# Optimization experiments

Hardware: AMD Instinct MI355X
Metric: run time of the kernel (lower is better)

## Reference

```python
import jax, jax.numpy as jnp
import numpy as np

L = 32768      # sequence length
H = 512        # n_features == d_model
P = 128        # state_size // 2 (conj_sym)
EPS = 1e-5     # haiku LayerNorm default eps


def setup_inputs() -> dict:
    key = jax.random.key(0)
    ks = jax.random.split(key, 10)
    x = jax.random.normal(ks[0], (L, H), dtype=jnp.float32)
    # S5 parameters (HiPPO-like init approximated with random values of same structure)
    lambda_real = -(0.1 + 0.5 * jax.random.uniform(ks[1], (P,), dtype=jnp.float32))
    lambda_imag = jnp.pi * jnp.arange(P, dtype=jnp.float32)
    b = jax.random.normal(ks[2], (P, H, 2), dtype=jnp.float32) / np.sqrt(H)
    c = jax.random.normal(ks[3], (H, P, 2), dtype=jnp.float32) / np.sqrt(2 * P)
    d = jax.random.normal(ks[4], (H,), dtype=jnp.float32)
    # log-uniform timescales in [1e-3, 1e-1]
    u = jax.random.uniform(ks[5], (P, 1), dtype=jnp.float32)
    delta = jnp.log(1e-3) + u * (jnp.log(1e-1) - jnp.log(1e-3))
    norm_scale = jnp.ones((H,), dtype=jnp.float32)
    norm_offset = jnp.zeros((H,), dtype=jnp.float32)
    w2 = jax.random.normal(ks[6], (H, H), dtype=jnp.float32) / np.sqrt(H)
    b2 = jnp.zeros((H,), dtype=jnp.float32)
    return {"x": x, "lambda_real": lambda_real, "lambda_imag": lambda_imag,
            "b": b, "c": c, "d": d, "delta": delta,
            "norm_scale": norm_scale, "norm_offset": norm_offset,
            "w2": w2, "b2": b2}


def _s5_block(x, lambda_real, lambda_imag, b, c, d, delta, norm_scale, norm_offset, w2, b2):
    skip = x
    # prenorm LayerNorm over last axis
    mean = jnp.mean(x, axis=-1, keepdims=True)
    var = jnp.var(x, axis=-1, keepdims=True)
    xn = (x - mean) * jax.lax.rsqrt(var + EPS) * norm_scale + norm_offset

    # --- S5 SSM ---
    lam = lambda_real + 1j * lambda_imag                      # [P]
    B = b[..., 0] + 1j * b[..., 1]                            # [P, H]
    C = c[..., 0] + 1j * c[..., 1]                            # [H, P]
    step = jnp.exp(delta[:, 0])                               # [P] (step_rescale = 1)
    # bilinear discretization
    bl = 1.0 / (1.0 - (step / 2.0) * lam)
    lam_bar = bl * (1.0 + (step / 2.0) * lam)                 # [P]
    B_bar = (bl * step)[:, None] * B                          # [P, H]

    Bu = jnp.einsum('lh,ph->lp', xn.astype(jnp.complex64), B_bar)  # [L, P]
    lam_elems = jnp.broadcast_to(lam_bar, (L, P))

    def binop(qi, qj):
        Ai, bi = qi
        Aj, bj = qj
        return Aj * Ai, Aj * bi + bj

    _, xs = jax.lax.associative_scan(binop, (lam_elems, Bu))  # states [L, P]
    # conj_sym: output is 2 * Re(C x)
    ys = 2.0 * jnp.einsum('lp,hp->lh', xs, C).real            # [L, H]
    y = ys + d * xn                                           # D skip term

    # half_glu2 (dropout_rate = 0 -> identity)
    x1 = jax.nn.gelu(y)
    out = y * jax.nn.sigmoid(x1 @ w2 + b2)
    return skip + out


def reference(x, lambda_real, lambda_imag, b, c, d, delta, norm_scale, norm_offset, w2, b2):
    return _s5_block(x, lambda_real, lambda_imag, b, c, d, delta,
                     norm_scale, norm_offset, w2, b2)
```

## Files before the change

### kernel.cpp

```cpp
#include <hip/hip_runtime.h>
#include <hip/hip_bf16.h>
#include <math.h>

#define LSEQ 32768
#define HF   512
#define PS   128
#define TWOP 256
#define NC   512
#define CL   64

typedef __attribute__((ext_vector_type(8))) short short8v;
typedef __attribute__((ext_vector_type(4))) float f32x4;

__device__ __forceinline__ float sig_fast(float z) {
    return __builtin_amdgcn_rcpf(1.0f + __expf(-z));
}
__device__ __forceinline__ float gelu_fast(float v) {
    float z = 1.5957691216057308f * v * fmaf(0.044715f, v * v, 1.0f);
    return v * sig_fast(z);
}
__device__ __forceinline__ unsigned short bf16bits(float f) {
    __hip_bfloat16 h = __float2bfloat16(f);
    return *(unsigned short*)&h;
}
__device__ __forceinline__ float bf2f(unsigned short u) {
    unsigned v = ((unsigned)u) << 16;
    return *(float*)&v;
}
__device__ __forceinline__ unsigned pk2(float a, float b) {
    return ((unsigned)bf16bits(b) << 16) | bf16bits(a);
}
__device__ __forceinline__ void gload_lds16(const void* g, void* l) {
    __builtin_amdgcn_global_load_lds(
        (const __attribute__((address_space(1))) unsigned int*)g,
        (__attribute__((address_space(3))) unsigned int*)l, 16, 0, 0);
}

__global__ __launch_bounds__(128) void prep_lam_k(
    const float* __restrict__ lr_, const float* __restrict__ li_,
    const float* __restrict__ delta, float* lam, float* bls, float* lamPow)
{
    int p = threadIdx.x;
    float lr = lr_[p], li = li_[p];
    float step = expf(delta[p]);
    float s2 = 0.5f * step;
    float dr = 1.0f - s2 * lr, di = -s2 * li;
    float inv = 1.0f / (dr * dr + di * di);
    float blr = dr * inv, bli = -di * inv;
    float nr = 1.0f + s2 * lr, ni = s2 * li;
    float lbr = blr * nr - bli * ni;
    float lbi = blr * ni + bli * nr;
    lam[2 * p] = lbr; lam[2 * p + 1] = lbi;
    bls[2 * p] = blr * step; bls[2 * p + 1] = bli * step;
    float pr = 1.0f, pim = 0.0f;
    lamPow[2 * p] = 1.0f; lamPow[2 * p + 1] = 0.0f;
    for (int k = 1; k <= CL; k++) {
        float t = pr * lbr - pim * lbi;
        pim = pr * lbi + pim * lbr;
        pr = t;
        lamPow[k * TWOP + 2 * p] = pr;
        lamPow[k * TWOP + 2 * p + 1] = pim;
    }
}

__global__ __launch_bounds__(256) void prep_B_k(
    const float* __restrict__ b, const float* __restrict__ bls,
    unsigned short* __restrict__ bwt)
{
    int idx = blockIdx.x * 256 + threadIdx.x;
    int p = idx >> 9, h = idx & 511;
    float2 bb = *(const float2*)(b + ((size_t)p * HF + h) * 2);
    float sr = bls[2 * p], si = bls[2 * p + 1];
    bwt[(size_t)(2 * p) * HF + h]     = bf16bits(sr * bb.x - si * bb.y);
    bwt[(size_t)(2 * p + 1) * HF + h] = bf16bits(sr * bb.y + si * bb.x);
}

__global__ __launch_bounds__(256) void prep_C_k(
    const float* __restrict__ c, unsigned short* __restrict__ cwt)
{
    int idx = blockIdx.x * 256 + threadIdx.x;
    int h = idx >> 7, p = idx & 127;
    float2 cc = *(const float2*)(c + ((size_t)h * PS + p) * 2);
    *(unsigned*)(cwt + (size_t)h * TWOP + 2 * p) = pk2(2.0f * cc.x, -2.0f * cc.y);
}

__global__ __launch_bounds__(256) void prep_w2_k(
    const float* __restrict__ w2, unsigned short* __restrict__ w2t)
{
    int idx = blockIdx.x * 256 + threadIdx.x;
    int n = idx >> 9, k = idx & 511;
    w2t[(size_t)n * HF + k] = bf16bits(w2[(size_t)k * HF + n]);
}

__global__ __launch_bounds__(128) void ln_k(
    const float* __restrict__ x, const float* __restrict__ scale,
    const float* __restrict__ offs, unsigned short* __restrict__ xnbf)
{
    int row = blockIdx.x, t = threadIdx.x;
    const float4* xr = (const float4*)(x + (size_t)row * HF);
    float4 v = xr[t];
    float s = v.x + v.y + v.z + v.w;
    float q = v.x * v.x + v.y * v.y + v.z * v.z + v.w * v.w;
    #pragma unroll
    for (int off = 32; off > 0; off >>= 1) {
        s += __shfl_down(s, off);
        q += __shfl_down(q, off);
    }
    __shared__ float ss[2], qq[2];
    if ((t & 63) == 0) { ss[t >> 6] = s; qq[t >> 6] = q; }
    __syncthreads();
    float S = ss[0] + ss[1], Q = qq[0] + qq[1];
    float mean = S * (1.0f / HF);
    float var = Q * (1.0f / HF) - mean * mean;
    float rstd = rsqrtf(var + 1e-5f);
    float4 sc = ((const float4*)scale)[t];
    float4 of = ((const float4*)offs)[t];
    ushort4 hv;
    hv.x = bf16bits((v.x - mean) * rstd * sc.x + of.x);
    hv.y = bf16bits((v.y - mean) * rstd * sc.y + of.y);
    hv.z = bf16bits((v.z - mean) * rstd * sc.z + of.z);
    hv.w = bf16bits((v.w - mean) * rstd * sc.w + of.w);
    ((ushort4*)(xnbf + (size_t)row * HF))[t] = hv;
}

__global__ __launch_bounds__(256) void g1scan_k(
    const unsigned short* __restrict__ A,
    const unsigned short* __restrict__ Bt,
    unsigned short* __restrict__ xs16,
    float* __restrict__ F,
    const float* __restrict__ lam)
{
    __shared__ float yt[128 * 128];
    unsigned short* As = (unsigned short*)yt;
    unsigned short* Bs = (unsigned short*)yt + 128 * 32;
    const int K = HF;
    int flat = (blockIdx.y << 1) + blockIdx.x;
    int f2 = (flat & 7) * 64 + (flat >> 3);
    const int bxi = f2 & 1, byi = f2 >> 1;
    const int bm = byi << 7;
    const int bn = bxi << 7;
    const int tid = threadIdx.x;
    const int lane = tid & 63;
    const int wid = tid >> 6;
    const int wr = wid >> 1, wc = wid & 1;

    f32x4 acc[4][4] = {};

    const int r0 = (wid << 5) + (lane >> 2);
    const int c0 = (lane & 3) << 3;
    const unsigned short* gA = A + (size_t)(bm + r0) * K + c0;
    const unsigned short* gB = Bt + (size_t)(bn + r0) * K + c0;
    unsigned short* lA0 = As + (wid << 5) * 32;
    unsigned short* lA1 = As + ((wid << 5) + 16) * 32;
    unsigned short* lB0 = Bs + (wid << 5) * 32;
    unsigned short* lB1 = Bs + ((wid << 5) + 16) * 32;
    const int aoff = ((wr << 6) + (lane & 15)) * 32 + ((lane >> 4) << 3);
    const int boff = ((wc << 6) + (lane & 15)) * 32 + ((lane >> 4) << 3);

    #pragma unroll
    for (int k0 = 0; k0 < HF; k0 += 32) {
        gload_lds16(gA + k0, lA0);
        gload_lds16(gA + k0 + (size_t)16 * K, lA1);
        gload_lds16(gB + k0, lB0);
        gload_lds16(gB + k0 + (size_t)16 * K, lB1);
        __syncthreads();
        short8v a[4], b[4];
        #pragma unroll
        for (int m = 0; m < 4; m++)
            a[m] = *(const short8v*)(As + aoff + (m << 4) * 32);
        #pragma unroll
        for (int n = 0; n < 4; n++)
            b[n] = *(const short8v*)(Bs + boff + (n << 4) * 32);
        #pragma unroll
        for (int m = 0; m < 4; m++)
            #pragma unroll
            for (int n = 0; n < 4; n++)
                acc[m][n] = __builtin_amdgcn_mfma_f32_16x16x32_bf16(
                    a[m], b[n], acc[m][n], 0, 0, 0);
        __syncthreads();
    }

    #pragma unroll
    for (int m = 0; m < 4; m++) {
        const int rowb = (wr << 6) + (m << 4) + ((lane >> 4) << 2);
        #pragma unroll
        for (int n = 0; n < 4; n++) {
            const int col = (wc << 6) + (n << 4) + (lane & 15);
            #pragma unroll
            for (int j = 0; j < 4; j++)
                yt[(rowb + j) * 128 + col] = acc[m][n][j];
        }
    }
    __syncthreads();

    if (tid < 128) {
        int ch = tid >> 6, q = tid & 63;
        int pg = (bxi << 6) + q;
        float lr = lam[2 * pg], liv = lam[2 * pg + 1];
        float sr = 0.0f, si = 0.0f;
        float* col = yt + (ch << 6) * 128 + 2 * q;
        #pragma unroll 8
        for (int i = 0; i < CL; i++) {
            float ur = col[i * 128], ui = col[i * 128 + 1];
            float tr = lr * sr - liv * si + ur;
            float ti = lr * si + liv * sr + ui;
            sr = tr; si = ti;
            col[i * 128] = sr; col[i * 128 + 1] = si;
        }
        int cg = (byi << 1) + ch;
        F[(size_t)cg * TWOP + (bxi << 7) + 2 * q] = sr;
        F[(size_t)cg * TWOP + (bxi << 7) + 2 * q + 1] = si;
    }
    __syncthreads();

    #pragma unroll
    for (int j = 0; j < 8; j++) {
        int fl = j * 256 + tid;
        int r = fl >> 4, ck = fl & 15;
        float4 v0 = *(float4*)&yt[r * 128 + ck * 8];
        float4 v1 = *(float4*)&yt[r * 128 + ck * 8 + 4];
        uint4 o;
        o.x = pk2(v0.x, v0.y); o.y = pk2(v0.z, v0.w);
        o.z = pk2(v1.x, v1.y); o.w = pk2(v1.z, v1.w);
        *(uint4*)(xs16 + (size_t)(bm + r) * TWOP + bn + ck * 8) = o;
    }
}

__global__ __launch_bounds__(512) void carry_k(
    const float* __restrict__ F, float* __restrict__ G,
    const float* __restrict__ lamPow)
{
    __shared__ float2 buf[NC];
    int c = threadIdx.x, p = blockIdx.x;
    float2 f = *(const float2*)(F + (size_t)c * TWOP + 2 * p);
    buf[c] = f;
    float aR = lamPow[CL * TWOP + 2 * p], aI = lamPow[CL * TWOP + 2 * p + 1];
    __syncthreads();
    #pragma unroll
    for (int d = 1; d < NC; d <<= 1) {
        bool act = (c >= d);
        float2 pv = act ? buf[c - d] : make_float2(0.0f, 0.0f);
        __syncthreads();
        if (act) {
            float2 cur = buf[c];
            cur.x += aR * pv.x - aI * pv.y;
            cur.y += aR * pv.y + aI * pv.x;
            buf[c] = cur;
        }
        __syncthreads();
        float nR = aR * aR - aI * aI;
        float nI = 2.0f * aR * aI;
        aR = nR; aI = nI;
    }
    *(float2*)(G + (size_t)c * TWOP + 2 * p) = buf[c];
}

__global__ __launch_bounds__(128) void fix_k(
    const unsigned short* __restrict__ xs16, const float* __restrict__ G,
    const float* __restrict__ lamPow, unsigned short* __restrict__ xsbf)
{
    int bc = blockIdx.x;
    int c = bc >> 2, qq = bc & 3;
    int p = threadIdx.x;
    float gr = 0.0f, gi = 0.0f;
    if (c > 0) {
        float2 g = *(const float2*)(G + (size_t)(c - 1) * TWOP + 2 * p);
        gr = g.x; gi = g.y;
    }
    size_t base = ((size_t)c * CL + (qq << 4)) * TWOP + 2 * p;
    #pragma unroll
    for (int i = 0; i < 16; i++) {
        float2 lp = *(const float2*)(lamPow + (size_t)((qq << 4) + i + 1) * TWOP + 2 * p);
        unsigned u = *(const unsigned*)(xs16 + base + (size_t)i * TWOP);
        float vr = bf2f((unsigned short)(u & 0xffff)) + lp.x * gr - lp.y * gi;
        float vi = bf2f((unsigned short)(u >> 16))    + lp.x * gi + lp.y * gr;
        *(unsigned*)(xsbf + base + (size_t)i * TWOP) = pk2(vr, vi);
    }
}

template<int MODE, int KT, int NT>
__global__ __launch_bounds__(256) void mgemm_k(
    const unsigned short* __restrict__ A, const unsigned short* __restrict__ Bt,
    const float* __restrict__ e0, const unsigned short* __restrict__ e1h,
    const float* __restrict__ e2, float* __restrict__ outF,
    unsigned short* __restrict__ o1, unsigned short* __restrict__ o2)
{
    __shared__ float smem[4224];
    unsigned short* As = (unsigned short*)smem;
    unsigned short* Bs = As + 128 * 32;
    float* eb = smem;

    constexpr int GX = NT >> 7;
    int flat = blockIdx.y * GX + blockIdx.x;
    constexpr int NWG = GX * (LSEQ >> 7);
    int f2 = (flat & 7) * (NWG >> 3) + (flat >> 3);
    const int bm = (f2 / GX) << 7;
    const int bn = (f2 % GX) << 7;

    const int tid = threadIdx.x;
    const int lane = tid & 63;
    const int wid = tid >> 6;
    const int wr = wid >> 1, wc = wid & 1;

    f32x4 acc[4][4] = {};

    const int r0 = (wid << 5) + (lane >> 2);
    const int c0 = (lane & 3) << 3;
    const unsigned short* gA = A + (size_t)(bm + r0) * KT + c0;
    const unsigned short* gB = Bt + (size_t)(bn + r0) * KT + c0;
    unsigned short* lA0 = As + (wid << 5) * 32;
    unsigned short* lA1 = As + ((wid << 5) + 16) * 32;
    unsigned short* lB0 = Bs + (wid << 5) * 32;
    unsigned short* lB1 = Bs + ((wid << 5) + 16) * 32;
    const int aoff = ((wr << 6) + (lane & 15)) * 32 + ((lane >> 4) << 3);
    const int boff = ((wc << 6) + (lane & 15)) * 32 + ((lane >> 4) << 3);

    #pragma unroll
    for (int k0 = 0; k0 < KT; k0 += 32) {
        gload_lds16(gA + k0, lA0);
        gload_lds16(gA + k0 + (size_t)16 * KT, lA1);
        gload_lds16(gB + k0, lB0);
        gload_lds16(gB + k0 + (size_t)16 * KT, lB1);
        __syncthreads();
        short8v a[4], b[4];
        #pragma unroll
        for (int m = 0; m < 4; m++)
            a[m] = *(const short8v*)(As + aoff + (m << 4) * 32);
        #pragma unroll
        for (int n = 0; n < 4; n++)
            b[n] = *(const short8v*)(Bs + boff + (n << 4) * 32);
        #pragma unroll
        for (int m = 0; m < 4; m++)
            #pragma unroll
            for (int n = 0; n < 4; n++)
                acc[m][n] = __builtin_amdgcn_mfma_f32_16x16x32_bf16(
                    a[m], b[n], acc[m][n], 0, 0, 0);
        __syncthreads();
    }

    #pragma unroll
    for (int p = 0; p < 4; p++) {
        if ((p >> 1) == wr) {
            const int mb = (p & 1) << 1;
            #pragma unroll
            for (int mm = 0; mm < 2; mm++) {
                const int lrow = (mm << 4) + ((lane >> 4) << 2);
                #pragma unroll
                for (int n = 0; n < 4; n++) {
                    const int col = (wc << 6) + (n << 4) + (lane & 15);
                    #pragma unroll
                    for (int j = 0; j < 4; j++)
                        eb[(lrow + j) * 132 + col] = acc[mb + mm][n][j];
                }
            }
        }
        __syncthreads();
        #pragma unroll
        for (int i = 0; i < 4; i++) {
            int idx = (i << 8) + tid;
            int row = idx >> 5, c4 = idx & 31;
            int gr = bm + (p << 5) + row;
            int gc = bn + (c4 << 2);
            size_t off = (size_t)gr * NT + gc;
            float4 v = *(float4*)&eb[row * 132 + (c4 << 2)];
            float4 e0v = *(const float4*)(e0 + gc);
            if (MODE == 1) {
                ushort4 xv = *(const ushort4*)(e1h + off);
                float y0 = v.x + e0v.x * bf2f(xv.x);
                float y1 = v.y + e0v.y * bf2f(xv.y);
                float y2 = v.z + e0v.z * bf2f(xv.z);
                float y3 = v.w + e0v.w * bf2f(xv.w);
                ushort4 a1, a2;
                a1.x = bf16bits(y0); a1.y = bf16bits(y1);
                a1.z = bf16bits(y2); a1.w = bf16bits(y3);
                a2.x = bf16bits(gelu_fast(y0)); a2.y = bf16bits(gelu_fast(y1));
                a2.z = bf16bits(gelu_fast(y2)); a2.w = bf16bits(gelu_fast(y3));
                *(ushort4*)(o1 + off) = a1;
                *(ushort4*)(o2 + off) = a2;
            } else {
                ushort4 yv = *(const ushort4*)(e1h + off);
                float4 xv = *(const float4*)(e2 + off);
                float4 o;
                o.x = xv.x + bf2f(yv.x) * sig_fast(v.x + e0v.x);
                o.y = xv.y + bf2f(yv.y) * sig_fast(v.y + e0v.y);
                o.z = xv.z + bf2f(yv.z) * sig_fast(v.z + e0v.z);
                o.w = xv.w + bf2f(yv.w) * sig_fast(v.w + e0v.w);
                *(float4*)(outF + off) = o;
            }
        }
        __syncthreads();
    }
}

extern "C" void kernel_launch(void* const* d_in, const int* in_sizes, int n_in,
                              void* d_out, int out_size, void* d_ws, size_t ws_size,
                              hipStream_t stream)
{
    const float* x      = (const float*)d_in[0];
    const float* lr     = (const float*)d_in[1];
    const float* li     = (const float*)d_in[2];
    const float* b      = (const float*)d_in[3];
    const float* c      = (const float*)d_in[4];
    const float* d      = (const float*)d_in[5];
    const float* delta  = (const float*)d_in[6];
    const float* nsc    = (const float*)d_in[7];
    const float* noff   = (const float*)d_in[8];
    const float* w2     = (const float*)d_in[9];
    const float* b2     = (const float*)d_in[10];
    float* out = (float*)d_out;

    unsigned short* XNBF = (unsigned short*)d_ws;
    unsigned short* YBF  = XNBF + (size_t)LSEQ * HF;
    unsigned short* XS16 = YBF + (size_t)LSEQ * HF;
    unsigned short* XSBF = XS16 + (size_t)LSEQ * TWOP;
    unsigned short* BWT  = XSBF + (size_t)LSEQ * TWOP;
    unsigned short* CWT  = BWT + (size_t)TWOP * HF;
    unsigned short* W2T  = CWT + (size_t)HF * TWOP;
    float* lam    = (float*)(W2T + (size_t)HF * HF);
    float* bls    = lam + TWOP;
    float* lamPow = bls + TWOP;
    float* F      = lamPow + (size_t)(CL + 1) * TWOP;
    float* G      = F + (size_t)NC * TWOP;

    prep_lam_k<<<1, 128, 0, stream>>>(lr, li, delta, lam, bls, lamPow);
    prep_B_k<<<(PS * HF) / 256, 256, 0, stream>>>(b, bls, BWT);
    prep_C_k<<<(HF * PS) / 256, 256, 0, stream>>>(c, CWT);
    prep_w2_k<<<(HF * HF) / 256, 256, 0, stream>>>(w2, W2T);
    ln_k<<<LSEQ, 128, 0, stream>>>(x, nsc, noff, XNBF);
    g1scan_k<<<dim3(TWOP >> 7, LSEQ >> 7), 256, 0, stream>>>(
        XNBF, BWT, XS16, F, lam);
    carry_k<<<PS, 512, 0, stream>>>(F, G, lamPow);
    fix_k<<<NC * 4, 128, 0, stream>>>(XS16, G, lamPow, XSBF);
    mgemm_k<1, TWOP, HF><<<dim3(4, LSEQ >> 7), 256, 0, stream>>>(
        XSBF, CWT, d, XNBF, nullptr, nullptr, YBF, XNBF);
    mgemm_k<2, HF, HF><<<dim3(4, LSEQ >> 7), 256, 0, stream>>>(
        XNBF, W2T, b2, YBF, x, out, nullptr, nullptr);
}
```

Measured before the change: 239.6 us.

## Double-buffer LDS tiles in GEMM main loops to overlap loads with MFMA

Both the Bu-scan GEMM and the generic mgemm kernel now keep two LDS stages. The next K-slice is prefetched with global_load_lds while the current slice is being multiplied, and each step ends with one vmcnt(0) wait plus a barrier instead of two syncthreads. The aim is to hide global-load latency behind MFMA work. The cost is a larger mgemm shared-memory footprint, 32KB versus about 17KB, which may lower occupancy. Correctness relies on the single barrier per step ordering the LDS reads of one buffer before that buffer is overwritten.

```diff
diff --git a/kernel.cpp b/kernel.cpp
--- a/kernel.cpp
+++ b/kernel.cpp
@@ -34,6 +34,10 @@
     __builtin_amdgcn_global_load_lds(
         (const __attribute__((address_space(1))) unsigned int*)g,
         (__attribute__((address_space(3))) unsigned int*)l, 16, 0, 0);
+}
+__device__ __forceinline__ void wait_vm0_barrier() {
+    asm volatile("s_waitcnt vmcnt(0)" ::: "memory");
+    __builtin_amdgcn_s_barrier();
 }
 
 __global__ __launch_bounds__(128) void prep_lam_k(
@@ -131,8 +135,7 @@
     const float* __restrict__ lam)
 {
     __shared__ float yt[128 * 128];
-    unsigned short* As = (unsigned short*)yt;
-    unsigned short* Bs = (unsigned short*)yt + 128 * 32;
+    unsigned short* Sb = (unsigned short*)yt;
     const int K = HF;
     int flat = (blockIdx.y << 1) + blockIdx.x;
     int f2 = (flat & 7) * 64 + (flat >> 3);
@@ -150,34 +153,41 @@
     const int c0 = (lane & 3) << 3;
     const unsigned short* gA = A + (size_t)(bm + r0) * K + c0;
     const unsigned short* gB = Bt + (size_t)(bn + r0) * K + c0;
-    unsigned short* lA0 = As + (wid << 5) * 32;
-    unsigned short* lA1 = As + ((wid << 5) + 16) * 32;
-    unsigned short* lB0 = Bs + (wid << 5) * 32;
-    unsigned short* lB1 = Bs + ((wid << 5) + 16) * 32;
+    const int stA0 = (wid << 5) * 32;
+    const int stA1 = ((wid << 5) + 16) * 32;
     const int aoff = ((wr << 6) + (lane & 15)) * 32 + ((lane >> 4) << 3);
     const int boff = ((wc << 6) + (lane & 15)) * 32 + ((lane >> 4) << 3);
 
-    #pragma unroll
-    for (int k0 = 0; k0 < HF; k0 += 32) {
-        gload_lds16(gA + k0, lA0);
-        gload_lds16(gA + k0 + (size_t)16 * K, lA1);
-        gload_lds16(gB + k0, lB0);
-        gload_lds16(gB + k0 + (size_t)16 * K, lB1);
-        __syncthreads();
-        short8v a[4], b[4];
-        #pragma unroll
-        for (int m = 0; m < 4; m++)
-            a[m] = *(const short8v*)(As + aoff + (m << 4) * 32);
-        #pragma unroll
-        for (int n = 0; n < 4; n++)
-            b[n] = *(const short8v*)(Bs + boff + (n << 4) * 32);
-        #pragma unroll
-        for (int m = 0; m < 4; m++)
-            #pragma unroll
-            for (int n = 0; n < 4; n++)
-                acc[m][n] = __builtin_amdgcn_mfma_f32_16x16x32_bf16(
-                    a[m], b[n], acc[m][n], 0, 0, 0);
-        __syncthreads();
+    #define G1_STAGE(b, k0) do { \
+        gload_lds16(gA + (k0), Sb + (b) * 8192 + stA0); \
+        gload_lds16(gA + (k0) + (size_t)16 * K, Sb + (b) * 8192 + stA1); \
+        gload_lds16(gB + (k0), Sb + (b) * 8192 + 4096 + stA0); \
+        gload_lds16(gB + (k0) + (size_t)16 * K, Sb + (b) * 8192 + 4096 + stA1); \
+    } while (0)
+    #define G1_COMPUTE(b) do { \
+        short8v a_[4], b_[4]; \
+        _Pragma("unroll") \
+        for (int m = 0; m < 4; m++) \
+            a_[m] = *(const short8v*)(Sb + (b) * 8192 + aoff + (m << 4) * 32); \
+        _Pragma("unroll") \
+        for (int n = 0; n < 4; n++) \
+            b_[n] = *(const short8v*)(Sb + (b) * 8192 + 4096 + boff + (n << 4) * 32); \
+        _Pragma("unroll") \
+        for (int m = 0; m < 4; m++) \
+            _Pragma("unroll") \
+            for (int n = 0; n < 4; n++) \
+                acc[m][n] = __builtin_amdgcn_mfma_f32_16x16x32_bf16( \
+                    a_[m], b_[n], acc[m][n], 0, 0, 0); \
+    } while (0)
+
+    G1_STAGE(0, 0);
+    wait_vm0_barrier();
+    #pragma unroll
+    for (int t = 0; t < 16; ++t) {
+        const int cur = t & 1;
+        if (t + 1 < 16) G1_STAGE(cur ^ 1, (t + 1) << 5);
+        G1_COMPUTE(cur);
+        wait_vm0_barrier();
     }
 
     #pragma unroll
@@ -285,9 +295,8 @@
     const float* __restrict__ e2, float* __restrict__ outF,
     unsigned short* __restrict__ o1, unsigned short* __restrict__ o2)
 {
-    __shared__ float smem[4224];
-    unsigned short* As = (unsigned short*)smem;
-    unsigned short* Bs = As + 128 * 32;
+    __shared__ float smem[8192];
+    unsigned short* Sb = (unsigned short*)smem;
     float* eb = smem;
 
     constexpr int GX = NT >> 7;
@@ -308,34 +317,42 @@
     const int c0 = (lane & 3) << 3;
     const unsigned short* gA = A + (size_t)(bm + r0) * KT + c0;
     const unsigned short* gB = Bt + (size_t)(bn + r0) * KT + c0;
-    unsigned short* lA0 = As + (wid << 5) * 32;
-    unsigned short* lA1 = As + ((wid << 5) + 16) * 32;
-    unsigned short* lB0 = Bs + (wid << 5) * 32;
-    unsigned short* lB1 = Bs + ((wid << 5) + 16) * 32;
+    const int stA0 = (wid << 5) * 32;
+    const int stA1 = ((wid << 5) + 16) * 32;
     const int aoff = ((wr << 6) + (lane & 15)) * 32 + ((lane >> 4) << 3);
     const int boff = ((wc << 6) + (lane & 15)) * 32 + ((lane >> 4) << 3);
-
-    #pragma unroll
-    for (int k0 = 0; k0 < KT; k0 += 32) {
-        gload_lds16(gA + k0, lA0);
-        gload_lds16(gA + k0 + (size_t)16 * KT, lA1);
-        gload_lds16(gB + k0, lB0);
-        gload_lds16(gB + k0 + (size_t)16 * KT, lB1);
-        __syncthreads();
-        short8v a[4], b[4];
-        #pragma unroll
-        for (int m = 0; m < 4; m++)
-            a[m] = *(const short8v*)(As + aoff + (m << 4) * 32);
-        #pragma unroll
-        for (int n = 0; n < 4; n++)
-            b[n] = *(const short8v*)(Bs + boff + (n << 4) * 32);
-        #pragma unroll
-        for (int m = 0; m < 4; m++)
-            #pragma unroll
-            for (int n = 0; n < 4; n++)
-                acc[m][n] = __builtin_amdgcn_mfma_f32_16x16x32_bf16(
-                    a[m], b[n], acc[m][n], 0, 0, 0);
-        __syncthreads();
+    constexpr int NSTEP = KT >> 5;
+
+    #define MG_STAGE(b, k0) do { \
+        gload_lds16(gA + (k0), Sb + (b) * 8192 + stA0); \
+        gload_lds16(gA + (k0) + (size_t)16 * KT, Sb + (b) * 8192 + stA1); \
+        gload_lds16(gB + (k0), Sb + (b) * 8192 + 4096 + stA0); \
+        gload_lds16(gB + (k0) + (size_t)16 * KT, Sb + (b) * 8192 + 4096 + stA1); \
+    } while (0)
+    #define MG_COMPUTE(b) do { \
+        short8v a_[4], b_[4]; \
+        _Pragma("unroll") \
+        for (int m = 0; m < 4; m++) \
+            a_[m] = *(const short8v*)(Sb + (b) * 8192 + aoff + (m << 4) * 32); \
+        _Pragma("unroll") \
+        for (int n = 0; n < 4; n++) \
+            b_[n] = *(const short8v*)(Sb + (b) * 8192 + 4096 + boff + (n << 4) * 32); \
+        _Pragma("unroll") \
+        for (int m = 0; m < 4; m++) \
+            _Pragma("unroll") \
+            for (int n = 0; n < 4; n++) \
+                acc[m][n] = __builtin_amdgcn_mfma_f32_16x16x32_bf16( \
+                    a_[m], b_[n], acc[m][n], 0, 0, 0); \
+    } while (0)
+
+    MG_STAGE(0, 0);
+    wait_vm0_barrier();
+    #pragma unroll
+    for (int t = 0; t < NSTEP; ++t) {
+        const int cur = t & 1;
+        if (t + 1 < NSTEP) MG_STAGE(cur ^ 1, (t + 1) << 5);
+        MG_COMPUTE(cur);
+        wait_vm0_barrier();
     }
 
     #pragma unroll
```

Result: no change. 236.6 us (-1.2%).
